# Performance work log

Hardware: AMD Instinct MI355X
Metric: run time of the kernel (lower is better)

Reference implementation:

```python
import jax, jax.numpy as jnp
import numpy as np

# BitLinear follows the BitNet b1.58 recipe used by fla's HGRN-Bit:
#   x -> RMSNorm(no weight) -> per-token int8 activation quant (STE)
#   w -> ternary quant with global mean-abs scale (STE)
#   out = x_q @ w_q.T

def _rms_norm(x, eps=1e-8, weight=None):
    var = jnp.mean(x * x, axis=-1, keepdims=True)
    y = x * jax.lax.rsqrt(var + eps)
    return y * weight if weight is not None else y


def _act_quant(x):
    # per-token absmax int8 quant-dequant with straight-through estimator
    scale = 127.0 / jnp.clip(jnp.max(jnp.abs(x), axis=-1, keepdims=True), 1e-5, None)
    q = jnp.clip(jnp.round(x * scale), -128, 127) / scale
    return x + jax.lax.stop_gradient(q - x)


def _weight_quant(w):
    # ternary {-1,0,1} quant-dequant with global mean-abs scale, STE
    scale = 1.0 / jnp.clip(jnp.mean(jnp.abs(w)), 1e-5, None)
    q = jnp.clip(jnp.round(w * scale), -1, 1) / scale
    return w + jax.lax.stop_gradient(q - w)


def _bit_linear(x, w):
    xq = _act_quant(_rms_norm(x))
    wq = _weight_quant(w)
    return jnp.einsum('...i,oi->...o', xq, wq)


def setup_inputs() -> dict:
    key = jax.random.key(0)
    ks = jax.random.split(key, 5)
    B, S = 2, 4096
    D_IN = 4096           # input_dim == 2 * hidden_size
    H = 2048              # hidden_size
    INTER = 2 * H         # HGRNBitMLP intermediate_size = hidden_size*2 = 4096
    condition = jax.random.normal(ks[0], (B, S, D_IN), dtype=jnp.float32)
    w_gate = jax.random.normal(ks[1], (2 * INTER, D_IN), dtype=jnp.float32) * 0.02   # [8192,4096]
    w_down = jax.random.normal(ks[2], (D_IN, INTER), dtype=jnp.float32) * 0.02        # [4096,4096]
    norm_weight = jnp.ones((2 * H,), dtype=jnp.float32)                                # RMSNorm(hidden_size*2)
    w_out = jax.random.normal(ks[3], (2 * H, 2 * H), dtype=jnp.float32) * 0.02         # [4096,4096]
    return {"condition": condition, "w_gate": w_gate, "w_down": w_down,
            "norm_weight": norm_weight, "w_out": w_out}


def reference(condition, w_gate, w_down, norm_weight, w_out):
    # HGRNBitMLP: gate_proj -> chunk -> swiglu -> down_proj
    y = _bit_linear(condition, w_gate)              # [B,S,8192]
    gate, v = jnp.split(y, 2, axis=-1)              # each [B,S,4096]
    h = _bit_linear(gate * jax.nn.sigmoid(gate) * v, w_down)  # swiglu then down, [B,S,4096]
    # AdaLN head: RMSNorm (learned weight) then quantized out projection
    h = _rms_norm(h, eps=1e-6, weight=norm_weight)
    params = _bit_linear(h, w_out)                  # [B,S,4096]
    scale, shift = jnp.split(params, 2, axis=-1)    # each [B,S,2048]
    return (scale, shift)
```

## Files before the change

kernel.cpp:

```cpp
#include <hip/hip_runtime.h>
#include <hip/hip_bf16.h>

typedef int i32x4 __attribute__((ext_vector_type(4)));
typedef signed char i8;


__device__ __forceinline__ void gload_lds16(const void* g, void* l) {
  __builtin_amdgcn_global_load_lds(
      (const __attribute__((address_space(1))) unsigned int*)g,
      (__attribute__((address_space(3))) unsigned int*)l, 16, 0, 0);
}

__device__ __forceinline__ float wmean_clip(const double* p, double cnt) {
  double m = *p / cnt;
  if (m < 1e-5) m = 1e-5;
  return (float)m;
}

__device__ __forceinline__ float blk_sum(float v, float* s4) {
  for (int m = 32; m; m >>= 1) v += __shfl_xor(v, m);
  if ((threadIdx.x & 63) == 0) s4[threadIdx.x >> 6] = v;
  __syncthreads();
  float r = s4[0] + s4[1] + s4[2] + s4[3];
  __syncthreads();
  return r;
}

__device__ __forceinline__ float blk_max(float v, float* s4) {
  for (int m = 32; m; m >>= 1) v = fmaxf(v, __shfl_xor(v, m));
  if ((threadIdx.x & 63) == 0) s4[threadIdx.x >> 6] = v;
  __syncthreads();
  float r = fmaxf(fmaxf(s4[0], s4[1]), fmaxf(s4[2], s4[3]));
  __syncthreads();
  return r;
}

__device__ __forceinline__ void xcd_swz(int gx, int& bm, int& bn) {
  const int nwg = gx * gridDim.y;
  const int o = blockIdx.y * gx + blockIdx.x;
  const int s = (o & 7) * (nwg >> 3) + (o >> 3);
  bm = s / gx;
  bn = s % gx;
}


__global__ __launch_bounds__(256) void wabs_reduce(
    const float* __restrict__ W, size_t n4, double* __restrict__ out) {
  __shared__ double s4[4];
  const float4* W4 = (const float4*)W;
  size_t i = (size_t)blockIdx.x * 256 + threadIdx.x;
  size_t stride = (size_t)gridDim.x * 256;
  double s = 0.0;
  for (; i < n4; i += stride) {
    float4 v = W4[i];
    s += (double)fabsf(v.x);
    s += (double)fabsf(v.y);
    s += (double)fabsf(v.z);
    s += (double)fabsf(v.w);
  }
  for (int m = 32; m; m >>= 1) s += __shfl_xor(s, m);
  if ((threadIdx.x & 63) == 0) s4[threadIdx.x >> 6] = s;
  __syncthreads();
  if (threadIdx.x == 0) atomicAdd(out, s4[0] + s4[1] + s4[2] + s4[3]);
}


__global__ __launch_bounds__(256) void wquant(
    const float* __restrict__ W, i8* __restrict__ Wq, size_t n4,
    const double* __restrict__ sum, double cnt) {
  float cm = wmean_clip(sum, cnt);
  float scale = 1.0f / cm;
  const float4* W4 = (const float4*)W;
  size_t i = (size_t)blockIdx.x * 256 + threadIdx.x;
  size_t stride = (size_t)gridDim.x * 256;
  for (; i < n4; i += stride) {
    float4 v = W4[i];
    char4 o;
    o.x = (i8)fminf(fmaxf(rintf(v.x * scale), -1.f), 1.f);
    o.y = (i8)fminf(fmaxf(rintf(v.y * scale), -1.f), 1.f);
    o.z = (i8)fminf(fmaxf(rintf(v.z * scale), -1.f), 1.f);
    o.w = (i8)fminf(fmaxf(rintf(v.w * scale), -1.f), 1.f);
    *(char4*)&Wq[i * 4] = o;
  }
}


template <bool HEAD>
__global__ __launch_bounds__(256) void rowquant(
    const float* __restrict__ X, const float* __restrict__ nw,
    i8* __restrict__ Aq, float* __restrict__ rowscale, float eps1) {
  __shared__ float s4[4];
  const int t = threadIdx.x;
  const size_t base = (size_t)blockIdx.x * 4096;
  float x[16];
#pragma unroll
  for (int c = 0; c < 4; ++c) {
    float4 v = *(const float4*)&X[base + c * 1024 + t * 4];
    x[c * 4 + 0] = v.x; x[c * 4 + 1] = v.y;
    x[c * 4 + 2] = v.z; x[c * 4 + 3] = v.w;
  }
  float ss = 0.f;
#pragma unroll
  for (int i = 0; i < 16; ++i) ss += x[i] * x[i];
  ss = blk_sum(ss, s4);
  float inv = 1.0f / sqrtf(ss * (1.0f / 4096.0f) + eps1);
  if (HEAD) {
#pragma unroll
    for (int c = 0; c < 4; ++c) {
      float4 w = *(const float4*)&nw[c * 1024 + t * 4];
      x[c * 4 + 0] = x[c * 4 + 0] * inv * w.x;
      x[c * 4 + 1] = x[c * 4 + 1] * inv * w.y;
      x[c * 4 + 2] = x[c * 4 + 2] * inv * w.z;
      x[c * 4 + 3] = x[c * 4 + 3] * inv * w.w;
    }
    float ss2 = 0.f;
#pragma unroll
    for (int i = 0; i < 16; ++i) ss2 += x[i] * x[i];
    ss2 = blk_sum(ss2, s4);
    inv = 1.0f / sqrtf(ss2 * (1.0f / 4096.0f) + 1e-8f);
  }
#pragma unroll
  for (int i = 0; i < 16; ++i) x[i] = x[i] * inv;
  float amax = 0.f;
#pragma unroll
  for (int i = 0; i < 16; ++i) amax = fmaxf(amax, fabsf(x[i]));
  amax = blk_max(amax, s4);
  float cs = fmaxf(amax, 1e-5f);
  float sx = 127.0f / cs;
#pragma unroll
  for (int c = 0; c < 4; ++c) {
    char4 o;
    o.x = (i8)fminf(fmaxf(rintf(x[c * 4 + 0] * sx), -128.f), 127.f);
    o.y = (i8)fminf(fmaxf(rintf(x[c * 4 + 1] * sx), -128.f), 127.f);
    o.z = (i8)fminf(fmaxf(rintf(x[c * 4 + 2] * sx), -128.f), 127.f);
    o.w = (i8)fminf(fmaxf(rintf(x[c * 4 + 3] * sx), -128.f), 127.f);
    *(char4*)&Aq[base + c * 1024 + t * 4] = o;
  }
  if (t == 0) rowscale[blockIdx.x] = cs / 127.0f;
}


__global__ __launch_bounds__(256) void gemm1_fused(
    const i8* __restrict__ A, const i8* __restrict__ Wg,
    float* __restrict__ SW, const float* __restrict__ rowscale,
    const double* __restrict__ wsum) {
  const int K = 4096;
  __shared__ i8 As[8192];
  __shared__ i8 Bg[4096];
  __shared__ i8 Bv[4096];
  const int t = threadIdx.x;
  int bmi, bni;
  xcd_swz(64, bmi, bni);
  const int bm0 = bmi * 128, bn0 = bni * 64;
  const int lane = t & 63, wave = t >> 6;
  const int wr = wave >> 1, wc = wave & 1;

  i32x4 accg[4][2] = {};
  i32x4 accv[4][2] = {};

  const i8* gA = A + (size_t)(bm0 + (t & 127)) * K + (t >> 7) * 16;
  const i8* gG = Wg + (size_t)(bn0 + (t & 63)) * K + (t >> 6) * 16;
  const i8* gV = Wg + (size_t)(4096 + bn0 + (t & 63)) * K + (t >> 6) * 16;
  i8* lA0 = As + t * 16;
  i8* lA1 = As + 4096 + t * 16;
  i8* lG = Bg + t * 16;
  i8* lV = Bv + t * 16;

  for (int kt = 0; kt < K; kt += 64) {
    gload_lds16(gA + kt, lA0);
    gload_lds16(gA + kt + 32, lA1);
    gload_lds16(gG + kt, lG);
    gload_lds16(gV + kt, lV);
    __syncthreads();
    const int ar = wr * 64 + (lane & 15);
    const int br = wc * 32 + (lane & 15);
    const int kcA = (lane >> 4) * 2048;
    const int kcB = (lane >> 4) * 1024;
    i32x4 af[4], bg[2], bv[2];
#pragma unroll
    for (int m = 0; m < 4; ++m) af[m] = *(const i32x4*)&As[kcA + (ar + m * 16) * 16];
#pragma unroll
    for (int n = 0; n < 2; ++n) {
      bg[n] = *(const i32x4*)&Bg[kcB + (br + n * 16) * 16];
      bv[n] = *(const i32x4*)&Bv[kcB + (br + n * 16) * 16];
    }
#pragma unroll
    for (int m = 0; m < 4; ++m)
#pragma unroll
      for (int n = 0; n < 2; ++n) {
        accg[m][n] = __builtin_amdgcn_mfma_i32_16x16x64_i8(af[m], bg[n], accg[m][n], 0, 0, 0);
        accv[m][n] = __builtin_amdgcn_mfma_i32_16x16x64_i8(af[m], bv[n], accv[m][n], 0, 0, 0);
      }
    __syncthreads();
  }

  const float cm = wmean_clip(wsum, 33554432.0);
#pragma unroll
  for (int m = 0; m < 4; ++m) {
    const int r0 = bm0 + wr * 64 + m * 16 + (lane >> 4) * 4;
#pragma unroll
    for (int j = 0; j < 4; ++j) {
      const int row = r0 + j;
      const float f = rowscale[row] * cm;
#pragma unroll
      for (int n = 0; n < 2; ++n) {
        const int col = bn0 + wc * 32 + n * 16 + (lane & 15);
        float g = (float)accg[m][n][j] * f;
        float v = (float)accv[m][n][j] * f;
        float s = g / (1.0f + expf(-g)) * v;
        SW[(size_t)row * 4096 + col] = s;
      }
    }
  }
}


template <int EPI>
__global__ __launch_bounds__(256) void gemm_bt(
    const i8* __restrict__ A, const i8* __restrict__ B,
    float* __restrict__ C, const float* __restrict__ rowscale,
    const double* __restrict__ wsum, double wcnt, int M) {
  const int K = 4096, N = 4096;
  __shared__ i8 As[8192];
  __shared__ i8 Bs[8192];
  const int t = threadIdx.x;
  int bmi, bni;
  xcd_swz(32, bmi, bni);
  const int bm0 = bmi * 128, bn0 = bni * 128;
  const int lane = t & 63, wave = t >> 6;
  const int wr = wave >> 1, wc = wave & 1;

  i32x4 acc[4][4] = {};

  const i8* gA = A + (size_t)(bm0 + (t & 127)) * K + (t >> 7) * 16;
  const i8* gB = B + (size_t)(bn0 + (t & 127)) * K + (t >> 7) * 16;
  i8* lA0 = As + t * 16;
  i8* lA1 = As + 4096 + t * 16;
  i8* lB0 = Bs + t * 16;
  i8* lB1 = Bs + 4096 + t * 16;

  for (int kt = 0; kt < K; kt += 64) {
    gload_lds16(gA + kt, lA0);
    gload_lds16(gA + kt + 32, lA1);
    gload_lds16(gB + kt, lB0);
    gload_lds16(gB + kt + 32, lB1);
    __syncthreads();
    const int ar = wr * 64 + (lane & 15);
    const int br = wc * 64 + (lane & 15);
    const int kc = (lane >> 4) * 2048;
    i32x4 af[4], bfr[4];
#pragma unroll
    for (int m = 0; m < 4; ++m) af[m] = *(const i32x4*)&As[kc + (ar + m * 16) * 16];
#pragma unroll
    for (int n = 0; n < 4; ++n) bfr[n] = *(const i32x4*)&Bs[kc + (br + n * 16) * 16];
#pragma unroll
    for (int m = 0; m < 4; ++m)
#pragma unroll
      for (int n = 0; n < 4; ++n)
        acc[m][n] = __builtin_amdgcn_mfma_i32_16x16x64_i8(af[m], bfr[n], acc[m][n], 0, 0, 0);
    __syncthreads();
  }

  const float cm = wmean_clip(wsum, wcnt);
#pragma unroll
  for (int m = 0; m < 4; ++m) {
    const int r0 = bm0 + wr * 64 + m * 16 + (lane >> 4) * 4;
#pragma unroll
    for (int j = 0; j < 4; ++j) {
      const int row = r0 + j;
      const float f = rowscale[row] * cm;
#pragma unroll
      for (int n = 0; n < 4; ++n) {
        const int col = bn0 + wc * 64 + n * 16 + (lane & 15);
        const float val = (float)acc[m][n][j] * f;
        if (EPI == 0) {
          C[(size_t)row * N + col] = val;
        } else {
          if (col < 2048)
            C[(size_t)row * 2048 + col] = val;
          else
            C[(size_t)M * 2048 + (size_t)row * 2048 + (col - 2048)] = val;
        }
      }
    }
  }
}


extern "C" void kernel_launch(void* const* d_in, const int* in_sizes, int n_in,
                              void* d_out, int out_size, void* d_ws, size_t ws_size,
                              hipStream_t stream) {
  const float* cond = (const float*)d_in[0];
  const float* w_gate = (const float*)d_in[1];
  const float* w_down = (const float*)d_in[2];
  const float* norm_w = (const float*)d_in[3];
  const float* w_out = (const float*)d_in[4];
  float* out = (float*)d_out;

  const int M = in_sizes[0] / 4096;

  char* ws = (char*)d_ws;
  double* sums = (double*)ws;
  i8* wq_gate = (i8*)(ws + 256);
  i8* wq_down = wq_gate + (size_t)8192 * 4096;
  i8* wq_out = wq_down + (size_t)4096 * 4096;
  i8* Aq = wq_out + (size_t)4096 * 4096;
  float* rowscale = (float*)(Aq + (size_t)M * 4096);
  float* act = rowscale + 8192;

  hipMemsetAsync(sums, 0, 3 * sizeof(double), stream);

  wabs_reduce<<<1024, 256, 0, stream>>>(w_gate, (size_t)8192 * 4096 / 4, &sums[0]);
  wabs_reduce<<<1024, 256, 0, stream>>>(w_down, (size_t)4096 * 4096 / 4, &sums[1]);
  wabs_reduce<<<1024, 256, 0, stream>>>(w_out, (size_t)4096 * 4096 / 4, &sums[2]);

  wquant<<<2048, 256, 0, stream>>>(w_gate, wq_gate, (size_t)8192 * 4096 / 4, &sums[0], 33554432.0);
  wquant<<<2048, 256, 0, stream>>>(w_down, wq_down, (size_t)4096 * 4096 / 4, &sums[1], 16777216.0);
  wquant<<<2048, 256, 0, stream>>>(w_out, wq_out, (size_t)4096 * 4096 / 4, &sums[2], 16777216.0);

  rowquant<false><<<M, 256, 0, stream>>>(cond, nullptr, Aq, rowscale, 1e-8f);
  gemm1_fused<<<dim3(4096 / 64, M / 128), 256, 0, stream>>>(Aq, wq_gate, act, rowscale, &sums[0]);

  rowquant<false><<<M, 256, 0, stream>>>(act, nullptr, Aq, rowscale, 1e-8f);
  gemm_bt<0><<<dim3(4096 / 128, M / 128), 256, 0, stream>>>(Aq, wq_down, act, rowscale, &sums[1], 16777216.0, M);

  rowquant<true><<<M, 256, 0, stream>>>(act, norm_w, Aq, rowscale, 1e-6f);
  gemm_bt<1><<<dim3(4096 / 128, M / 128), 256, 0, stream>>>(Aq, wq_out, out, rowscale, &sums[2], 16777216.0, M);
}
```

Measured before the change: 1.630 ms.

## Double-buffer LDS in int8 GEMMs and merge weight reduce/quant launches

Both int8 GEMM kernels now keep two LDS buffers and issue the global-to-LDS loads for the next K tile before computing on the current one, so load latency can overlap MFMA work. The per-tensor weight abs-sum and ternary quant kernels are merged into one launch each covering all three weights, cutting four kernel launches. Double buffering doubles LDS use per block, which may lower occupancy. The prefetch into the alternate buffer relies on the end-of-iteration barrier, and its correctness also depends on async LDS loads being waited on before that barrier.

```diff
diff --git a/kernel.cpp b/kernel.cpp
--- a/kernel.cpp
+++ b/kernel.cpp
@@ -44,12 +44,19 @@
 }
 
 
-__global__ __launch_bounds__(256) void wabs_reduce(
-    const float* __restrict__ W, size_t n4, double* __restrict__ out) {
+__global__ __launch_bounds__(256) void wabs_all(
+    const float* __restrict__ W0, const float* __restrict__ W1,
+    const float* __restrict__ W2, double* __restrict__ sums) {
   __shared__ double s4[4];
-  const float4* W4 = (const float4*)W;
-  size_t i = (size_t)blockIdx.x * 256 + threadIdx.x;
-  size_t stride = (size_t)gridDim.x * 256;
+  const int b = blockIdx.x;
+  const float4* W4;
+  size_t n4;
+  int rb, nb, r;
+  if (b < 1024) { r = 0; rb = b; nb = 1024; W4 = (const float4*)W0; n4 = (size_t)8192 * 1024; }
+  else if (b < 1536) { r = 1; rb = b - 1024; nb = 512; W4 = (const float4*)W1; n4 = (size_t)4096 * 1024; }
+  else { r = 2; rb = b - 1536; nb = 512; W4 = (const float4*)W2; n4 = (size_t)4096 * 1024; }
+  size_t i = (size_t)rb * 256 + threadIdx.x;
+  size_t stride = (size_t)nb * 256;
   double s = 0.0;
   for (; i < n4; i += stride) {
     float4 v = W4[i];
@@ -61,18 +68,26 @@
   for (int m = 32; m; m >>= 1) s += __shfl_xor(s, m);
   if ((threadIdx.x & 63) == 0) s4[threadIdx.x >> 6] = s;
   __syncthreads();
-  if (threadIdx.x == 0) atomicAdd(out, s4[0] + s4[1] + s4[2] + s4[3]);
-}
-
-
-__global__ __launch_bounds__(256) void wquant(
-    const float* __restrict__ W, i8* __restrict__ Wq, size_t n4,
-    const double* __restrict__ sum, double cnt) {
-  float cm = wmean_clip(sum, cnt);
-  float scale = 1.0f / cm;
-  const float4* W4 = (const float4*)W;
-  size_t i = (size_t)blockIdx.x * 256 + threadIdx.x;
-  size_t stride = (size_t)gridDim.x * 256;
+  if (threadIdx.x == 0) atomicAdd(&sums[r], s4[0] + s4[1] + s4[2] + s4[3]);
+}
+
+
+__global__ __launch_bounds__(256) void wquant_all(
+    const float* __restrict__ W0, const float* __restrict__ W1,
+    const float* __restrict__ W2, i8* __restrict__ Q0, i8* __restrict__ Q1,
+    i8* __restrict__ Q2, const double* __restrict__ sums) {
+  const int b = blockIdx.x;
+  const float4* W4;
+  i8* Q;
+  size_t n4;
+  int rb, nb, r;
+  double cnt;
+  if (b < 2048) { r = 0; rb = b; nb = 2048; W4 = (const float4*)W0; Q = Q0; n4 = (size_t)8192 * 1024; cnt = 33554432.0; }
+  else if (b < 3072) { r = 1; rb = b - 2048; nb = 1024; W4 = (const float4*)W1; Q = Q1; n4 = (size_t)4096 * 1024; cnt = 16777216.0; }
+  else { r = 2; rb = b - 3072; nb = 1024; W4 = (const float4*)W2; Q = Q2; n4 = (size_t)4096 * 1024; cnt = 16777216.0; }
+  const float scale = 1.0f / wmean_clip(&sums[r], cnt);
+  size_t i = (size_t)rb * 256 + threadIdx.x;
+  size_t stride = (size_t)nb * 256;
   for (; i < n4; i += stride) {
     float4 v = W4[i];
     char4 o;
@@ -80,7 +95,7 @@
     o.y = (i8)fminf(fmaxf(rintf(v.y * scale), -1.f), 1.f);
     o.z = (i8)fminf(fmaxf(rintf(v.z * scale), -1.f), 1.f);
     o.w = (i8)fminf(fmaxf(rintf(v.w * scale), -1.f), 1.f);
-    *(char4*)&Wq[i * 4] = o;
+    *(char4*)&Q[i * 4] = o;
   }
 }
 
@@ -145,9 +160,9 @@
     float* __restrict__ SW, const float* __restrict__ rowscale,
     const double* __restrict__ wsum) {
   const int K = 4096;
-  __shared__ i8 As[8192];
-  __shared__ i8 Bg[4096];
-  __shared__ i8 Bv[4096];
+  __shared__ i8 As[2][8192];
+  __shared__ i8 Bg[2][4096];
+  __shared__ i8 Bv[2][4096];
   const int t = threadIdx.x;
   int bmi, bni;
   xcd_swz(64, bmi, bni);
@@ -161,28 +176,32 @@
   const i8* gA = A + (size_t)(bm0 + (t & 127)) * K + (t >> 7) * 16;
   const i8* gG = Wg + (size_t)(bn0 + (t & 63)) * K + (t >> 6) * 16;
   const i8* gV = Wg + (size_t)(4096 + bn0 + (t & 63)) * K + (t >> 6) * 16;
-  i8* lA0 = As + t * 16;
-  i8* lA1 = As + 4096 + t * 16;
-  i8* lG = Bg + t * 16;
-  i8* lV = Bv + t * 16;
-
+
+  auto stage = [&](int buf, int kt) {
+    gload_lds16(gA + kt, &As[buf][t * 16]);
+    gload_lds16(gA + kt + 32, &As[buf][4096 + t * 16]);
+    gload_lds16(gG + kt, &Bg[buf][t * 16]);
+    gload_lds16(gV + kt, &Bv[buf][t * 16]);
+  };
+
+  stage(0, 0);
+  __syncthreads();
+
+  const int ar = wr * 64 + (lane & 15);
+  const int br = wc * 32 + (lane & 15);
+  const int kcA = (lane >> 4) * 2048;
+  const int kcB = (lane >> 4) * 1024;
+
+  int cur = 0;
   for (int kt = 0; kt < K; kt += 64) {
-    gload_lds16(gA + kt, lA0);
-    gload_lds16(gA + kt + 32, lA1);
-    gload_lds16(gG + kt, lG);
-    gload_lds16(gV + kt, lV);
-    __syncthreads();
-    const int ar = wr * 64 + (lane & 15);
-    const int br = wc * 32 + (lane & 15);
-    const int kcA = (lane >> 4) * 2048;
-    const int kcB = (lane >> 4) * 1024;
+    if (kt + 64 < K) stage(cur ^ 1, kt + 64);
     i32x4 af[4], bg[2], bv[2];
 #pragma unroll
-    for (int m = 0; m < 4; ++m) af[m] = *(const i32x4*)&As[kcA + (ar + m * 16) * 16];
+    for (int m = 0; m < 4; ++m) af[m] = *(const i32x4*)&As[cur][kcA + (ar + m * 16) * 16];
 #pragma unroll
     for (int n = 0; n < 2; ++n) {
-      bg[n] = *(const i32x4*)&Bg[kcB + (br + n * 16) * 16];
-      bv[n] = *(const i32x4*)&Bv[kcB + (br + n * 16) * 16];
+      bg[n] = *(const i32x4*)&Bg[cur][kcB + (br + n * 16) * 16];
+      bv[n] = *(const i32x4*)&Bv[cur][kcB + (br + n * 16) * 16];
     }
 #pragma unroll
     for (int m = 0; m < 4; ++m)
@@ -192,6 +211,7 @@
         accv[m][n] = __builtin_amdgcn_mfma_i32_16x16x64_i8(af[m], bv[n], accv[m][n], 0, 0, 0);
       }
     __syncthreads();
+    cur ^= 1;
   }
 
   const float cm = wmean_clip(wsum, 33554432.0);
@@ -221,8 +241,8 @@
     float* __restrict__ C, const float* __restrict__ rowscale,
     const double* __restrict__ wsum, double wcnt, int M) {
   const int K = 4096, N = 4096;
-  __shared__ i8 As[8192];
-  __shared__ i8 Bs[8192];
+  __shared__ i8 As[2][8192];
+  __shared__ i8 Bs[2][8192];
   const int t = threadIdx.x;
   int bmi, bni;
   xcd_swz(32, bmi, bni);
@@ -234,31 +254,36 @@
 
   const i8* gA = A + (size_t)(bm0 + (t & 127)) * K + (t >> 7) * 16;
   const i8* gB = B + (size_t)(bn0 + (t & 127)) * K + (t >> 7) * 16;
-  i8* lA0 = As + t * 16;
-  i8* lA1 = As + 4096 + t * 16;
-  i8* lB0 = Bs + t * 16;
-  i8* lB1 = Bs + 4096 + t * 16;
-
+
+  auto stage = [&](int buf, int kt) {
+    gload_lds16(gA + kt, &As[buf][t * 16]);
+    gload_lds16(gA + kt + 32, &As[buf][4096 + t * 16]);
+    gload_lds16(gB + kt, &Bs[buf][t * 16]);
+    gload_lds16(gB + kt + 32, &Bs[buf][4096 + t * 16]);
+  };
+
+  stage(0, 0);
+  __syncthreads();
+
+  const int ar = wr * 64 + (lane & 15);
+  const int br = wc * 64 + (lane & 15);
+  const int kc = (lane >> 4) * 2048;
+
+  int cur = 0;
   for (int kt = 0; kt < K; kt += 64) {
-    gload_lds16(gA + kt, lA0);
-    gload_lds16(gA + kt + 32, lA1);
-    gload_lds16(gB + kt, lB0);
-    gload_lds16(gB + kt + 32, lB1);
-    __syncthreads();
-    const int ar = wr * 64 + (lane & 15);
-    const int br = wc * 64 + (lane & 15);
-    const int kc = (lane >> 4) * 2048;
+    if (kt + 64 < K) stage(cur ^ 1, kt + 64);
     i32x4 af[4], bfr[4];
 #pragma unroll
-    for (int m = 0; m < 4; ++m) af[m] = *(const i32x4*)&As[kc + (ar + m * 16) * 16];
-#pragma unroll
-    for (int n = 0; n < 4; ++n) bfr[n] = *(const i32x4*)&Bs[kc + (br + n * 16) * 16];
+    for (int m = 0; m < 4; ++m) af[m] = *(const i32x4*)&As[cur][kc + (ar + m * 16) * 16];
+#pragma unroll
+    for (int n = 0; n < 4; ++n) bfr[n] = *(const i32x4*)&Bs[cur][kc + (br + n * 16) * 16];
 #pragma unroll
     for (int m = 0; m < 4; ++m)
 #pragma unroll
       for (int n = 0; n < 4; ++n)
         acc[m][n] = __builtin_amdgcn_mfma_i32_16x16x64_i8(af[m], bfr[n], acc[m][n], 0, 0, 0);
     __syncthreads();
+    cur ^= 1;
   }
 
   const float cm = wmean_clip(wsum, wcnt);
@@ -310,13 +335,8 @@
 
   hipMemsetAsync(sums, 0, 3 * sizeof(double), stream);
 
-  wabs_reduce<<<1024, 256, 0, stream>>>(w_gate, (size_t)8192 * 4096 / 4, &sums[0]);
-  wabs_reduce<<<1024, 256, 0, stream>>>(w_down, (size_t)4096 * 4096 / 4, &sums[1]);
-  wabs_reduce<<<1024, 256, 0, stream>>>(w_out, (size_t)4096 * 4096 / 4, &sums[2]);
-
-  wquant<<<2048, 256, 0, stream>>>(w_gate, wq_gate, (size_t)8192 * 4096 / 4, &sums[0], 33554432.0);
-  wquant<<<2048, 256, 0, stream>>>(w_down, wq_down, (size_t)4096 * 4096 / 4, &sums[1], 16777216.0);
-  wquant<<<2048, 256, 0, stream>>>(w_out, wq_out, (size_t)4096 * 4096 / 4, &sums[2], 16777216.0);
+  wabs_all<<<2048, 256, 0, stream>>>(w_gate, w_down, w_out, sums);
+  wquant_all<<<4096, 256, 0, stream>>>(w_gate, w_down, w_out, wq_gate, wq_down, wq_out, sums);
 
   rowquant<false><<<M, 256, 0, stream>>>(cond, nullptr, Aq, rowscale, 1e-8f);
   gemm1_fused<<<dim3(4096 / 64, M / 128), 256, 0, stream>>>(Aq, wq_gate, act, rowscale, &sums[0]);
```

Measured after the change: 1.639 ms. About the same (+0.6%).
